# Performance work log

Measured on AMD Instinct MI355X. Metric: run time of the kernel, lower is better.

Reference implementation:

```python
import jax, jax.numpy as jnp
import numpy as np
import math

B, S, D = 4, 2048, 1024
H, HD, L = 16, 64, 512
ROPE_BASE = 10000.0
EPS = 1e-6


def _rope_angles(seq_len, head_dim, base):
    # (seq_len, head_dim//2) rotation angles
    inv_freq = 1.0 / (base ** (jnp.arange(0, head_dim, 2, dtype=jnp.float32) / head_dim))
    pos = jnp.arange(seq_len, dtype=jnp.float32)
    return pos[:, None] * inv_freq[None, :]


def _apply_rope(t, ang):
    # t: (B, H, S, HD); half-split rotation (rotate-half convention)
    cos = jnp.cos(ang)  # (S, HD//2)
    sin = jnp.sin(ang)
    t1, t2 = jnp.split(t, 2, axis=-1)
    return jnp.concatenate([t1 * cos - t2 * sin, t1 * sin + t2 * cos], axis=-1)


def setup_inputs() -> dict:
    key = jax.random.key(0)
    ks = jax.random.split(key, 7)
    def w(k, shape, fan_in):
        return jax.random.normal(k, shape, jnp.float32) * (fan_in ** -0.5)
    return {
        "x": jax.random.normal(ks[0], (B, S, D), jnp.float32),
        "norm_w": jnp.ones((D,), jnp.float32),
        "wq": w(ks[1], (D, H * HD), D),
        "kv_down": w(ks[2], (D, L), D),
        "wk": w(ks[3], (L, H * HD), L),
        "wv": w(ks[4], (L, H * HD), L),
        "wo": w(ks[5], (H * HD, D), H * HD),
    }


def reference(x, norm_w, wq, kv_down, wk, wv, wo):
    residual = x
    # RMSNorm
    var = jnp.mean(x * x, axis=-1, keepdims=True)
    xn = x * jax.lax.rsqrt(var + EPS) * norm_w
    # Projections: q from full x, k/v from latent down-projection
    q = (xn @ wq).reshape(B, S, H, HD).transpose(0, 2, 1, 3)          # (B,H,S,HD)
    kv = xn @ kv_down                                                  # (B,S,L)
    k = (kv @ wk).reshape(B, S, H, HD).transpose(0, 2, 1, 3)
    v = (kv @ wv).reshape(B, S, H, HD).transpose(0, 2, 1, 3)
    # RoPE
    ang = _rope_angles(S, HD, ROPE_BASE)
    q = _apply_rope(q, ang)
    k = _apply_rope(k, ang)
    # Attention (full, no mask)
    scale = 1.0 / math.sqrt(HD)
    attn = jnp.einsum("bhsd,bhtd->bhst", q, k) * scale
    attn = jax.nn.softmax(attn, axis=-1)
    out = jnp.einsum("bhst,bhtd->bhsd", attn, v)
    out = out.transpose(0, 2, 1, 3).reshape(B, S, H * HD) @ wo
    return residual + out
```

## Files before the change

### kernel.cpp

```cpp
#include <hip/hip_runtime.h>

typedef unsigned short u16;
typedef unsigned int   u32;
typedef __attribute__((ext_vector_type(8)))  __bf16 bf16x8;
typedef __attribute__((ext_vector_type(2)))  __bf16 bf16x2;
typedef __attribute__((ext_vector_type(8)))  short  short8;
typedef __attribute__((ext_vector_type(4)))  float  f32x4;
typedef __attribute__((ext_vector_type(16))) float  f32x16;
typedef __attribute__((ext_vector_type(4)))  u16    u16x4;
typedef __attribute__((ext_vector_type(4)))  u32    u32x4;

#define DEV static __device__ __forceinline__

DEV u16 f2bf(float f){ return __builtin_bit_cast(u16, (__bf16)f); }
DEV u32 pkbf(float a, float b){ bf16x2 t; t[0] = (__bf16)a; t[1] = (__bf16)b;
                                return __builtin_bit_cast(u32, t); }

#if __has_builtin(__builtin_amdgcn_exp2f)
DEV float fexp2(float x){ return __builtin_amdgcn_exp2f(x); }
#else
DEV float fexp2(float x){ return exp2f(x); }
#endif

DEV f32x4 mfma16(short8 a, short8 b, f32x4 c){
  return __builtin_amdgcn_mfma_f32_16x16x32_bf16(
      __builtin_bit_cast(bf16x8, a), __builtin_bit_cast(bf16x8, b), c, 0, 0, 0);
}
DEV f32x16 mfma32(short8 a, short8 b, f32x16 c){
  return __builtin_amdgcn_mfma_f32_32x32x16_bf16(
      __builtin_bit_cast(bf16x8, a), __builtin_bit_cast(bf16x8, b), c, 0, 0, 0);
}
DEV int swz(int byteoff, int row){ return byteoff ^ ((row & 7) << 4); }

#if __has_builtin(__builtin_amdgcn_global_load_lds)
#define USE_GLL 1
typedef __attribute__((address_space(1))) const u32 gas_u32;
typedef __attribute__((address_space(3)))       u32 las_u32;
#define GL2L(g, l) __builtin_amdgcn_global_load_lds((gas_u32*)(g), (las_u32*)(l), 16, 0, 0)
#define LSWZ(boff, r) swz(boff, r)
#else
#define LSWZ(boff, r) (boff)
#endif

__global__ __launch_bounds__(256) void k_prep(const float* __restrict__ wq,
                                              const float* __restrict__ kvd,
                                              const float* __restrict__ wk,
                                              const float* __restrict__ wv,
                                              const float* __restrict__ wo,
                                              const float* __restrict__ x,
                                              const float* __restrict__ norm_w,
                                              u16* __restrict__ wqT, u16* __restrict__ kvdT,
                                              u16* __restrict__ wkT, u16* __restrict__ wvT,
                                              u16* __restrict__ woT, u16* __restrict__ xn,
                                              float2* __restrict__ cs, float qscale){
  const int z = blockIdx.z;
  if (z == 6){
    const int bid = blockIdx.y*32 + blockIdx.x;
    const int t = threadIdx.x;
    __shared__ float ps[4];
    const float4 g = ((const float4*)norm_w)[t];
    #pragma unroll 1
    for (int it = 0; it < 8; ++it){
      const int row = bid*8 + it;
      const float4 v = ((const float4*)(x + (size_t)row*1024))[t];
      float ss = v.x*v.x + v.y*v.y + v.z*v.z + v.w*v.w;
      #pragma unroll
      for (int off=32; off; off>>=1) ss += __shfl_xor(ss, off, 64);
      if ((t & 63) == 0) ps[t>>6] = ss;
      __syncthreads();
      const float tot = ps[0]+ps[1]+ps[2]+ps[3];
      const float rinv = rsqrtf(tot * (1.0f/1024.0f) + 1e-6f);
      u16x4 o;
      o.x = f2bf(v.x*rinv*g.x); o.y = f2bf(v.y*rinv*g.y);
      o.z = f2bf(v.z*rinv*g.z); o.w = f2bf(v.w*rinv*g.w);
      *(u16x4*)(xn + (size_t)row*1024 + t*4) = o;
      __syncthreads();
    }
    return;
  }
  if (z == 5){
    if (blockIdx.y >= 8) return;
    const int idx = (blockIdx.y*32 + blockIdx.x)*256 + threadIdx.x;
    const int s = idx >> 5, j = idx & 31;
    const float ang = (float)s * expf(-(float)j * (9.210340371976184f/32.0f));
    cs[idx] = make_float2(cosf(ang), sinf(ang));
    return;
  }
  const float* W; u16* Wt; int K, N; float sc = 1.0f;
  switch (z){
    case 0: W = wq;  Wt = wqT;  K = 1024; N = 1024; sc = qscale; break;
    case 1: W = kvd; Wt = kvdT; K = 1024; N = 512;  break;
    case 2: W = wk;  Wt = wkT;  K = 512;  N = 1024; break;
    case 3: W = wv;  Wt = wvT;  K = 512;  N = 1024; break;
    default: W = wo; Wt = woT;  K = 1024; N = 1024; break;
  }
  const int k0 = blockIdx.x*32, n0 = blockIdx.y*32;
  if (k0 >= K || n0 >= N) return;
  __shared__ float t[32][33];
  const int tx = threadIdx.x & 31, ty = threadIdx.x >> 5;
  #pragma unroll
  for (int j=0;j<4;++j) t[ty + j*8][tx] = W[(size_t)(k0+ty+j*8)*N + n0 + tx];
  __syncthreads();
  #pragma unroll
  for (int j=0;j<4;++j) Wt[(size_t)(n0+ty+j*8)*K + k0 + tx] = f2bf(t[tx][ty+j*8]*sc);
}

template<int MODE>
__global__ __launch_bounds__(256) void k_gemm(const u16* __restrict__ A,
                                              const u16* __restrict__ Bt,
                                              const u16* __restrict__ Bt2,
                                              u16* __restrict__ Cb,
                                              u16* __restrict__ Cb2,
                                              float* __restrict__ Cf,
                                              const float* __restrict__ resid,
                                              const float2* __restrict__ cs,
                                              int K){
  __shared__ __align__(16) u16 Al[2][128*64];
  __shared__ __align__(16) u16 Bl[2][128*64];
  const int tid = threadIdx.x, lane = tid & 63, w = tid >> 6;
  const int wm = (w >> 1) * 64, wn = (w & 1) * 64;

  const int gx = gridDim.x;
  const int nwg = gx * gridDim.y;
  int fid = blockIdx.y * gx + blockIdx.x;
  fid = (fid & 7) * (nwg >> 3) + (fid >> 3);
  const int bx = fid % gx, by = fid / gx;

  const bool second = (MODE != 2) && (bx >= 8);
  const u16* B = second ? Bt2 : Bt;
  const int n0 = (second ? bx - 8 : bx) * 128;
  const int m0 = by * 128;
  const int lr = lane & 15, lg = lane >> 4;
  const int nt = K >> 6;

  f32x4 acc[4][4] = {};

#ifdef USE_GLL
  const int rin  = lane >> 3;
  const int colq = (lane & 7) ^ rin;
  auto stage = [&](int t_){
    u16* Ad = &Al[t_ & 1][0];
    u16* Bd = &Bl[t_ & 1][0];
    const int kb = t_ << 6;
    #pragma unroll
    for (int j=0;j<4;++j){
      const int c = w*4 + j;
      GL2L(A + (size_t)(m0 + c*8 + rin)*K + kb + colq*8, Ad + c*512);
      GL2L(B + (size_t)(n0 + c*8 + rin)*K + kb + colq*8, Bd + c*512);
    }
  };
#else
  auto stage = [&](int t_){
    u16* Ad = &Al[t_ & 1][0];
    u16* Bd = &Bl[t_ & 1][0];
    const int kb = t_ << 6;
    const int srow = tid >> 1, scol = (tid & 1) * 32;
    #pragma unroll
    for (int j=0;j<4;++j){
      *(short8*)(Ad + srow*64 + scol + j*8) = *(const short8*)(A + (size_t)(m0+srow)*K + kb + scol + j*8);
      *(short8*)(Bd + srow*64 + scol + j*8) = *(const short8*)(B + (size_t)(n0+srow)*K + kb + scol + j*8);
    }
  };
#endif

  stage(0);
  for (int t = 0; t < nt; ++t){
    __syncthreads();
    if (t + 1 < nt) stage(t + 1);
    const u16* Ab = &Al[t & 1][0];
    const u16* Bb = &Bl[t & 1][0];
    #pragma unroll
    for (int kk=0; kk<2; ++kk){
      const int cb = kk*64 + lg*16;
      short8 af[4], bfr[4];
      #pragma unroll
      for (int m=0;m<4;++m){
        const int r = wm + m*16 + lr;
        af[m] = *(const short8*)((const char*)Ab + LSWZ(r*128 + cb, r));
      }
      #pragma unroll
      for (int n=0;n<4;++n){
        const int r = wn + n*16 + lr;
        bfr[n] = *(const short8*)((const char*)Bb + LSWZ(r*128 + cb, r));
      }
      #pragma unroll
      for (int m=0;m<4;++m)
        #pragma unroll
        for (int n=0;n<4;++n)
          acc[m][n] = mfma16(af[m], bfr[n], acc[m][n]);
    }
  }

  #pragma unroll
  for (int m=0;m<4;++m){
    const int rb = m0 + wm + m*16 + lg*4;
    if (MODE == 2){
      #pragma unroll
      for (int n=0;n<4;++n){
        const int c = n0 + wn + n*16 + lr;
        #pragma unroll
        for (int i=0;i<4;++i){
          const size_t off = (size_t)(rb+i)*1024 + c;
          Cf[off] = acc[m][n][i] + resid[off];
        }
      }
    } else if (!second){
      #pragma unroll
      for (int n=0;n<2;++n){
        const int c = n0 + wn + n*16 + lr;
        const int j = n*16 + lr;
        #pragma unroll
        for (int i=0;i<4;++i){
          const float2 t = cs[(size_t)((rb+i) & 2047)*32 + j];
          const float t1 = acc[m][n][i], t2 = acc[m][n+2][i];
          Cb[(size_t)(rb+i)*1024 + c]      = f2bf(t1*t.x - t2*t.y);
          Cb[(size_t)(rb+i)*1024 + c + 32] = f2bf(t1*t.y + t2*t.x);
        }
      }
    } else if (MODE == 4){
      #pragma unroll
      for (int n=0;n<4;++n){
        const int c = n0 + wn + n*16 + lr;
        #pragma unroll
        for (int i=0;i<4;++i) Cb2[(size_t)(rb+i)*512 + c] = f2bf(acc[m][n][i]);
      }
    } else {
      #pragma unroll
      for (int n=0;n<4;++n){
        const int c = n0 + wn + n*16 + lr;
        const int b = rb >> 11, s = rb & 2047;
        u16x4 pk;
        pk.x = f2bf(acc[m][n][0]); pk.y = f2bf(acc[m][n][1]);
        pk.z = f2bf(acc[m][n][2]); pk.w = f2bf(acc[m][n][3]);
        *(u16x4*)(Cb2 + (((size_t)(b*1024 + c)) << 11) + s) = pk;
      }
    }
  }
}

__global__ __launch_bounds__(256, 3) void k_attn(const u16* __restrict__ q,
                                                 const u16* __restrict__ kmat,
                                                 const u16* __restrict__ vT,
                                                 u16* __restrict__ o){
  __shared__ __align__(16) u16 Kl[2][64*64];
  __shared__ __align__(16) u16 Vl[2][64*64];
  const int tid = threadIdx.x, lane = tid & 63, w = tid >> 6;
  const int l31 = lane & 31, hi = lane >> 5;

  const int fid = blockIdx.y * 16 + blockIdx.x;
  const int sid = (fid & 7) * 128 + (fid >> 3);
  const int qx = sid & 15, bh = sid >> 4;
  const int b = bh >> 4, h = bh & 15;
  const int q0 = qx * 128;

  short8 qf[4];
  {
    const size_t base = ((size_t)(b*2048 + q0 + w*32 + l31) << 10) + (h<<6) + hi*8;
    qf[0] = *(const short8*)(q + base);
    qf[1] = *(const short8*)(q + base + 16);
    qf[2] = *(const short8*)(q + base + 32);
    qf[3] = *(const short8*)(q + base + 48);
  }
  f32x16 oacc0 = {}, oacc1 = {};
  float m = -1e30f, l = 0.f;

  int roff[8];
  #pragma unroll
  for (int c=0;c<4;++c){
    roff[c*2+0] = swz(l31*128      + c*32 + hi*16, l31);
    roff[c*2+1] = swz((32+l31)*128 + c*32 + hi*16, 32+l31);
  }

  const int rin  = lane >> 3;
  const int colq = (lane & 7) ^ rin;
  const u16* kp0 = kmat + ((size_t)(b*2048 + w*16 + rin) << 10) + (h<<6) + colq*8;
  const u16* kp1 = kp0 + ((size_t)8 << 10);
  const u16* vp0 = vT + (((size_t)(b*1024 + h*64 + w*16 + rin)) << 11) + colq*8;
  const u16* vp1 = vp0 + ((size_t)8 << 11);
  u16* const Kd0 = Kl[0] + w*1024;  u16* const Kd1 = Kl[1] + w*1024;
  u16* const Vd0 = Vl[0] + w*1024;  u16* const Vd1 = Vl[1] + w*1024;

#ifdef USE_GLL
  #define STAGE(KD, VD) { GL2L(kp0, KD); GL2L(kp1, KD + 512);                   \
      GL2L(vp0, VD); GL2L(vp1, VD + 512);                                       \
      kp0 += 65536; kp1 += 65536; vp0 += 64; vp1 += 64; }
#else
  #define STAGE(KD, VD) { *(short8*)(KD + lane*8) = *(const short8*)(kp0);      \
      *(short8*)(KD + 512 + lane*8) = *(const short8*)(kp1);                    \
      *(short8*)(VD + lane*8) = *(const short8*)(vp0);                          \
      *(short8*)(VD + 512 + lane*8) = *(const short8*)(vp1);                    \
      kp0 += 65536; kp1 += 65536; vp0 += 64; vp1 += 64; }
#endif

  #define TILE(BOFF) {                                                          \
    f32x16 s0 = {}, s1 = {};                                                    \
    __builtin_amdgcn_s_setprio(1);                                              \
    _Pragma("unroll")                                                           \
    for (int c=0;c<4;++c){                                                      \
      short8 kf0 = *(const short8*)((const char*)Kl + roff[c*2+0] + BOFF);      \
      short8 kf1 = *(const short8*)((const char*)Kl + roff[c*2+1] + BOFF);      \
      s0 = mfma32(kf0, qf[c], s0);                                              \
      s1 = mfma32(kf1, qf[c], s1);                                              \
    }                                                                           \
    __builtin_amdgcn_s_setprio(0);                                              \
    float tmax = fmaxf(s0[0], s0[1]);                                           \
    _Pragma("unroll")                                                           \
    for (int r=1;r<8;++r) tmax = fmaxf(fmaxf(tmax, s0[2*r]), s0[2*r+1]);        \
    _Pragma("unroll")                                                           \
    for (int r=0;r<8;++r) tmax = fmaxf(fmaxf(tmax, s1[2*r]), s1[2*r+1]);        \
    tmax = fmaxf(tmax, __shfl_xor(tmax, 32, 64));                               \
    if (__any(tmax > m + 8.0f)){                                                \
      const float mn = fmaxf(m, tmax);                                          \
      const float corr = fexp2(m - mn);                                         \
      m = mn; l *= corr;                                                        \
      _Pragma("unroll")                                                         \
      for (int reg=0; reg<16; ++reg){                                           \
        const int cq = (reg&3) + 8*(reg>>2) + 4*hi;                             \
        const float cr = __shfl(corr, cq, 64);                                  \
        oacc0[reg] *= cr; oacc1[reg] *= cr;                                     \
      }                                                                         \
    }                                                                           \
    float rs0 = 0.f, rs1 = 0.f;                                                 \
    u32 pk0[8], pk1[8];                                                         \
    _Pragma("unroll")                                                           \
    for (int a=0;a<4;++a){                                                      \
      _Pragma("unroll")                                                         \
      for (int e=0;e<2;++e){                                                    \
        float pa = fexp2(s0[a*4+e*2] - m), pb = fexp2(s0[a*4+e*2+1] - m);       \
        rs0 += pa + pb;  pk0[a*2+e] = pkbf(pa, pb);                             \
        pa = fexp2(s1[a*4+e*2] - m); pb = fexp2(s1[a*4+e*2+1] - m);             \
        rs1 += pa + pb;  pk1[a*2+e] = pkbf(pa, pb);                             \
      }                                                                         \
    }                                                                           \
    float rs = rs0 + rs1;                                                       \
    rs += __shfl_xor(rs, 32, 64);                                               \
    l += rs;                                                                    \
    __builtin_amdgcn_s_setprio(1);                                              \
    _Pragma("unroll")                                                           \
    for (int c=0;c<4;++c){                                                      \
      u32* pks = (c < 2) ? pk0 : pk1;                                           \
      const int cc = c & 1;                                                     \
      u32 a0 = pks[(2*cc)*2+0], b0 = pks[(2*cc+1)*2+0];                         \
      u32 a1 = pks[(2*cc)*2+1], b1 = pks[(2*cc+1)*2+1];                         \
      asm volatile("v_permlane32_swap_b32 %0, %1" : "+v"(a0), "+v"(b0));        \
      asm volatile("v_permlane32_swap_b32 %0, %1" : "+v"(a1), "+v"(b1));        \
      u32x4 pfv; pfv.x = a0; pfv.y = a1; pfv.z = b0; pfv.w = b1;                \
      const short8 pf = __builtin_bit_cast(short8, pfv);                        \
      short8 vf0 = *(const short8*)((const char*)Vl + roff[c*2+0] + BOFF);      \
      short8 vf1 = *(const short8*)((const char*)Vl + roff[c*2+1] + BOFF);      \
      oacc0 = mfma32(pf, vf0, oacc0);                                           \
      oacc1 = mfma32(pf, vf1, oacc1);                                           \
    }                                                                           \
    __builtin_amdgcn_s_setprio(0);                                              \
  }

  STAGE(Kd0, Vd0);
  #pragma unroll 1
  for (int tt = 0; tt < 16; ++tt){
    __syncthreads();
    STAGE(Kd1, Vd1);
    TILE(0);
    __syncthreads();
    if (tt < 15) STAGE(Kd0, Vd0);
    TILE(8192);
  }

  const float linv = 1.0f / l;
  #pragma unroll
  for (int reg=0; reg<16; ++reg){
    const int cq = (reg&3) + 8*(reg>>2) + 4*hi;
    const float lv = __shfl(linv, cq, 64);
    const size_t rowbase = ((size_t)(b*2048 + q0 + w*32 + cq) << 10) + (h<<6);
    o[rowbase + l31]      = f2bf(oacc0[reg] * lv);
    o[rowbase + 32 + l31] = f2bf(oacc1[reg] * lv);
  }
  #undef STAGE
  #undef TILE
}

extern "C" void kernel_launch(void* const* d_in, const int* in_sizes, int n_in,
                              void* d_out, int out_size, void* d_ws, size_t ws_size,
                              hipStream_t stream){
  const float* x      = (const float*)d_in[0];
  const float* norm_w = (const float*)d_in[1];
  const float* wq     = (const float*)d_in[2];
  const float* kvd    = (const float*)d_in[3];
  const float* wk     = (const float*)d_in[4];
  const float* wv     = (const float*)d_in[5];
  const float* wo     = (const float*)d_in[6];
  float* out = (float*)d_out;

  char* ws = (char*)d_ws;
  const size_t SZ = (size_t)8192*1024*2;
  u16* xn   = (u16*)(ws);
  u16* q    = (u16*)(ws + SZ);
  u16* kmat = (u16*)(ws + 2*SZ);
  u16* vT   = (u16*)(ws + 3*SZ);
  u16* attn = (u16*)(ws + 4*SZ);
  u16* kv   = (u16*)(ws + 5*SZ);
  u16* wqT  = (u16*)(ws + 5*SZ + (size_t)8192*512*2);
  u16* kvdT = wqT  + 1024*1024;
  u16* wkT  = kvdT + 512*1024;
  u16* wvT  = wkT  + 1024*512;
  u16* woT  = wvT  + 1024*512;
  float2* cs = (float2*)(woT + 1024*1024);

  const float QSCALE = 0.125f * 1.4426950408889634f;

  k_prep<<<dim3(32,32,7), 256, 0, stream>>>(wq, kvd, wk, wv, wo, x, norm_w,
                                            wqT, kvdT, wkT, wvT, woT, xn, cs, QSCALE);

  k_gemm<4><<<dim3(12,64), 256, 0, stream>>>(xn, wqT, kvdT, q, kv, nullptr, nullptr, cs, 1024);
  k_gemm<5><<<dim3(16,64), 256, 0, stream>>>(kv, wkT, wvT, kmat, vT, nullptr, nullptr, cs, 512);

  k_attn<<<dim3(16,64), 256, 0, stream>>>(q, kmat, vT, attn);

  k_gemm<2><<<dim3(8,64), 256, 0, stream>>>(attn, woT, nullptr, nullptr, nullptr, out, x, nullptr, 1024);
}
```

Measured before the change: 201.0 us.

## Triple-buffer K/V in attention and software-pipeline QK^T one tile ahead

The attention kernel moves from double- to triple-buffered K/V LDS tiles. It computes the next tile's QK^T before running softmax and PV on the current tile, so matrix-core work can overlap the exp/max arithmetic, and it drops to one barrier per tile. Cross-half reductions now use v_permlane32_swap instead of shuffles, and launch bounds drop from 3 to 2 blocks per CU to make room for the extra registers and LDS. The cost is lower occupancy, more register pressure, and a more complex prologue and epilogue.

```diff
diff --git a/kernel.cpp b/kernel.cpp
--- a/kernel.cpp
+++ b/kernel.cpp
@@ -238,12 +238,12 @@
   }
 }
 
-__global__ __launch_bounds__(256, 3) void k_attn(const u16* __restrict__ q,
+__global__ __launch_bounds__(256, 2) void k_attn(const u16* __restrict__ q,
                                                  const u16* __restrict__ kmat,
                                                  const u16* __restrict__ vT,
                                                  u16* __restrict__ o){
-  __shared__ __align__(16) u16 Kl[2][64*64];
-  __shared__ __align__(16) u16 Vl[2][64*64];
+  __shared__ __align__(16) u16 Kl[3][64*64];
+  __shared__ __align__(16) u16 Vl[3][64*64];
   const int tid = threadIdx.x, lane = tid & 63, w = tid >> 6;
   const int l31 = lane & 31, hi = lane >> 5;
 
@@ -277,38 +277,43 @@
   const u16* kp1 = kp0 + ((size_t)8 << 10);
   const u16* vp0 = vT + (((size_t)(b*1024 + h*64 + w*16 + rin)) << 11) + colq*8;
   const u16* vp1 = vp0 + ((size_t)8 << 11);
-  u16* const Kd0 = Kl[0] + w*1024;  u16* const Kd1 = Kl[1] + w*1024;
-  u16* const Vd0 = Vl[0] + w*1024;  u16* const Vd1 = Vl[1] + w*1024;
 
 #ifdef USE_GLL
-  #define STAGE(KD, VD) { GL2L(kp0, KD); GL2L(kp1, KD + 512);                   \
+  #define STAGE(CUR) { u16* KD = (u16*)((char*)Kl + (CUR)*8192) + w*1024;       \
+      u16* VD = (u16*)((char*)Vl + (CUR)*8192) + w*1024;                        \
+      GL2L(kp0, KD); GL2L(kp1, KD + 512);                                       \
       GL2L(vp0, VD); GL2L(vp1, VD + 512);                                       \
       kp0 += 65536; kp1 += 65536; vp0 += 64; vp1 += 64; }
 #else
-  #define STAGE(KD, VD) { *(short8*)(KD + lane*8) = *(const short8*)(kp0);      \
+  #define STAGE(CUR) { u16* KD = (u16*)((char*)Kl + (CUR)*8192) + w*1024;       \
+      u16* VD = (u16*)((char*)Vl + (CUR)*8192) + w*1024;                        \
+      *(short8*)(KD + lane*8) = *(const short8*)(kp0);                          \
       *(short8*)(KD + 512 + lane*8) = *(const short8*)(kp1);                    \
       *(short8*)(VD + lane*8) = *(const short8*)(vp0);                          \
       *(short8*)(VD + 512 + lane*8) = *(const short8*)(vp1);                    \
       kp0 += 65536; kp1 += 65536; vp0 += 64; vp1 += 64; }
 #endif
 
-  #define TILE(BOFF) {                                                          \
-    f32x16 s0 = {}, s1 = {};                                                    \
+  #define QKT(NXT, N0, N1) {                                                    \
     __builtin_amdgcn_s_setprio(1);                                              \
     _Pragma("unroll")                                                           \
     for (int c=0;c<4;++c){                                                      \
-      short8 kf0 = *(const short8*)((const char*)Kl + roff[c*2+0] + BOFF);      \
-      short8 kf1 = *(const short8*)((const char*)Kl + roff[c*2+1] + BOFF);      \
-      s0 = mfma32(kf0, qf[c], s0);                                              \
-      s1 = mfma32(kf1, qf[c], s1);                                              \
+      short8 kf0 = *(const short8*)((const char*)Kl + roff[c*2+0] + (NXT)*8192);\
+      short8 kf1 = *(const short8*)((const char*)Kl + roff[c*2+1] + (NXT)*8192);\
+      N0 = mfma32(kf0, qf[c], N0);                                              \
+      N1 = mfma32(kf1, qf[c], N1);                                              \
     }                                                                           \
-    __builtin_amdgcn_s_setprio(0);                                              \
+    __builtin_amdgcn_s_setprio(0); }
+
+  #define SMAX_PV(CUR) {                                                        \
     float tmax = fmaxf(s0[0], s0[1]);                                           \
     _Pragma("unroll")                                                           \
     for (int r=1;r<8;++r) tmax = fmaxf(fmaxf(tmax, s0[2*r]), s0[2*r+1]);        \
     _Pragma("unroll")                                                           \
     for (int r=0;r<8;++r) tmax = fmaxf(fmaxf(tmax, s1[2*r]), s1[2*r+1]);        \
-    tmax = fmaxf(tmax, __shfl_xor(tmax, 32, 64));                               \
+    { u32 ta = __builtin_bit_cast(u32, tmax), tb = ta;                          \
+      asm volatile("v_permlane32_swap_b32 %0, %1" : "+v"(ta), "+v"(tb));        \
+      tmax = fmaxf(__builtin_bit_cast(float, ta), __builtin_bit_cast(float, tb)); } \
     if (__any(tmax > m + 8.0f)){                                                \
       const float mn = fmaxf(m, tmax);                                          \
       const float corr = fexp2(m - mn);                                         \
@@ -332,9 +337,10 @@
         rs1 += pa + pb;  pk1[a*2+e] = pkbf(pa, pb);                             \
       }                                                                         \
     }                                                                           \
-    float rs = rs0 + rs1;                                                       \
-    rs += __shfl_xor(rs, 32, 64);                                               \
-    l += rs;                                                                    \
+    { float rsx = rs0 + rs1;                                                    \
+      u32 ra = __builtin_bit_cast(u32, rsx), rb = ra;                           \
+      asm volatile("v_permlane32_swap_b32 %0, %1" : "+v"(ra), "+v"(rb));        \
+      l += __builtin_bit_cast(float, ra) + __builtin_bit_cast(float, rb); }     \
     __builtin_amdgcn_s_setprio(1);                                              \
     _Pragma("unroll")                                                           \
     for (int c=0;c<4;++c){                                                      \
@@ -346,24 +352,39 @@
       asm volatile("v_permlane32_swap_b32 %0, %1" : "+v"(a1), "+v"(b1));        \
       u32x4 pfv; pfv.x = a0; pfv.y = a1; pfv.z = b0; pfv.w = b1;                \
       const short8 pf = __builtin_bit_cast(short8, pfv);                        \
-      short8 vf0 = *(const short8*)((const char*)Vl + roff[c*2+0] + BOFF);      \
-      short8 vf1 = *(const short8*)((const char*)Vl + roff[c*2+1] + BOFF);      \
+      short8 vf0 = *(const short8*)((const char*)Vl + roff[c*2+0] + (CUR)*8192);\
+      short8 vf1 = *(const short8*)((const char*)Vl + roff[c*2+1] + (CUR)*8192);\
       oacc0 = mfma32(pf, vf0, oacc0);                                           \
       oacc1 = mfma32(pf, vf1, oacc1);                                           \
     }                                                                           \
-    __builtin_amdgcn_s_setprio(0);                                              \
-  }
-
-  STAGE(Kd0, Vd0);
+    __builtin_amdgcn_s_setprio(0); }
+
+  #define BODY(CUR, NXT, DOSTAGE) {                                             \
+    f32x16 n0 = {}, n1 = {};                                                    \
+    QKT(NXT, n0, n1)                                                            \
+    SMAX_PV(CUR)                                                                \
+    __syncthreads();                                                            \
+    if (DOSTAGE) STAGE(CUR);                                                    \
+    s0 = n0; s1 = n1; }
+
+  STAGE(0); STAGE(1); STAGE(2);
+  __syncthreads();
+  f32x16 s0 = {}, s1 = {};
+  QKT(0, s0, s1)
+
   #pragma unroll 1
-  for (int tt = 0; tt < 16; ++tt){
-    __syncthreads();
-    STAGE(Kd1, Vd1);
-    TILE(0);
-    __syncthreads();
-    if (tt < 15) STAGE(Kd0, Vd0);
-    TILE(8192);
-  }
+  for (int u = 0; u < 10; ++u){
+    BODY(0, 1, true)
+    BODY(1, 2, true)
+    BODY(2, 0, (u < 9))
+  }
+  {
+    f32x16 n0 = {}, n1 = {};
+    QKT(1, n0, n1)
+    SMAX_PV(0)
+    s0 = n0; s1 = n1;
+  }
+  SMAX_PV(1)
 
   const float linv = 1.0f / l;
   #pragma unroll
@@ -375,7 +396,9 @@
     o[rowbase + 32 + l31] = f2bf(oacc1[reg] * lv);
   }
   #undef STAGE
-  #undef TILE
+  #undef QKT
+  #undef SMAX_PV
+  #undef BODY
 }
 
 extern "C" void kernel_launch(void* const* d_in, const int* in_sizes, int n_in,
```

Measured after the change: 193.3 us. -3.9%, faster.
